# Performance work log

Hardware: AMD Instinct MI355X
Metric: run time of the kernel (lower is better)

## Reference

```python
import jax, jax.numpy as jnp
import numpy as np

B = 64          # batch
N_IN = 1_000_000  # SNPs (n_inputs)
N_OUT = 20_000    # genes (n_outputs = mask.shape[1])
KMAX = 64         # filter_size = max SNPs per gene


def setup_inputs() -> dict:
    key = jax.random.key(0)
    k1, k2, k3, k4 = jax.random.split(key, 4)
    x = jax.random.normal(k1, (B, N_IN), dtype=jnp.float32)
    kernel = jax.random.normal(k2, (KMAX, N_OUT), dtype=jnp.float32) * 0.05
    bias = jnp.zeros((N_OUT, 1), dtype=jnp.float32)
    # static COO mask encoded as padded per-gene index table + valid lengths
    gather_idx = jax.random.randint(k3, (N_OUT, KMAX), 0, N_IN, dtype=jnp.int32)
    lengths = jax.random.randint(k4, (N_OUT,), 1, KMAX + 1, dtype=jnp.int32)
    return {"x": x, "kernel": kernel, "bias": bias,
            "gather_idx": gather_idx, "lengths": lengths}


def reference(x, kernel, bias, gather_idx, lengths):
    # valid[g,k] = 1 if slot k of gene g holds a real SNP (padding mask)
    valid = (jnp.arange(KMAX, dtype=lengths.dtype)[None, :] < lengths[:, None])
    # per-gene weights, zeroed at padded slots: (G, K)
    w = jnp.where(valid, kernel.T, jnp.zeros((), dtype=kernel.dtype))
    # gather inputs per gene group: (B, G, K)
    gathered = x[:, gather_idx]
    # grouped multiply-reduce: (B, G)
    out = jnp.einsum('bgk,gk->bg', gathered, w)
    # bias per (gene, filter), filters = 1 -> output (B, G, 1)
    out = out[..., None] + bias[None, :, :]
    return out  # linear activation
```

## Files before the change

### kernel.cpp

```cpp
#include <hip/hip_runtime.h>
#include <hip/hip_bf16.h>

#define B_DIM 64
#define N_IN 1000000
#define N_OUT 20000
#define KMAX 64
#define GPB 16

__global__ __launch_bounds__(256) void zero_flags(uint4* __restrict__ f) {
    int tid = blockIdx.x * 256 + threadIdx.x;
    if (tid < N_IN / 16) f[tid] = uint4{0, 0, 0, 0};
}

__global__ __launch_bounds__(256) void build_flags(
    const int* __restrict__ gidx, const int* __restrict__ lengths,
    unsigned char* __restrict__ flags) {
    int tid = blockIdx.x * 256 + threadIdx.x;
    int g = tid >> 6, k = tid & 63;
    if (g < N_OUT && k < lengths[g]) flags[gidx[g * KMAX + k]] = 1;
    if (tid == 0) flags[0] = 1;
}

__global__ __launch_bounds__(256) void transpose_x_bf16_masked(
    const float* __restrict__ src, __hip_bfloat16* __restrict__ dst,
    const unsigned char* __restrict__ flags) {
    __shared__ float ldsT[64 * 65];
    __shared__ unsigned char f[64];
    const int t  = threadIdx.x;
    const int c0 = blockIdx.x * 64;
    if (t < 64) f[t] = flags[c0 + t];
    const int col4 = (t & 15) * 4;
    const int r0   = t >> 4;
#pragma unroll
    for (int i = 0; i < 4; ++i) {
        int r = r0 + 16 * i;
        float4 v = *reinterpret_cast<const float4*>(&src[(size_t)r * N_IN + c0 + col4]);
        ldsT[(col4 + 0) * 65 + r] = v.x;
        ldsT[(col4 + 1) * 65 + r] = v.y;
        ldsT[(col4 + 2) * 65 + r] = v.z;
        ldsT[(col4 + 3) * 65 + r] = v.w;
    }
    __syncthreads();
    const int half = t & 31;
    const int cb   = t >> 5;
#pragma unroll
    for (int i = 0; i < 8; ++i) {
        int c = cb + 8 * i;
        if (f[c]) {
            __hip_bfloat162 h2;
            h2.x = __float2bfloat16(ldsT[c * 65 + half * 2]);
            h2.y = __float2bfloat16(ldsT[c * 65 + half * 2 + 1]);
            *reinterpret_cast<__hip_bfloat162*>(&dst[(size_t)(c0 + c) * 64 + half * 2]) = h2;
        }
    }
}

__global__ __launch_bounds__(256) void transpose_64xC_f32(
    const float* __restrict__ src, float* __restrict__ dst, int C) {
    __shared__ float lds[64 * 65];
    const int c0 = blockIdx.x * 64;
    const int t  = threadIdx.x;
    const int cq = t & 63;
    const int rq = t >> 6;
#pragma unroll
    for (int i = 0; i < 16; ++i) {
        int r = i * 4 + rq;
        int c = c0 + cq;
        if (c < C) lds[r * 65 + cq] = src[r * C + c];
    }
    __syncthreads();
#pragma unroll
    for (int i = 0; i < 16; ++i) {
        int c = i * 4 + rq;
        int r = cq;
        if (c0 + c < C) dst[(c0 + c) * 64 + r] = lds[r * 65 + c];
    }
}

__global__ __launch_bounds__(1024) void gather_dot_fused(
    const __hip_bfloat16* __restrict__ xT,
    const float* __restrict__ wT,
    const int*   __restrict__ gidx,
    const int*   __restrict__ lengths,
    const float* __restrict__ bias,
    float*       __restrict__ out) {
    __shared__ float sm[64 * 17];
    const int wave = threadIdx.x >> 6;
    const int lane = threadIdx.x & 63;
    const int g0   = blockIdx.x * GPB;
    const int g    = g0 + wave;

    const int len = lengths[g];
    const int   idx_l = (lane < len) ? gidx[g * KMAX + lane] : 0;
    const float w_l   = (lane < len) ? wT[g * KMAX + lane] : 0.0f;

    float acc = 0.0f;
    for (int k = 0; k < len; k += 4) {
        int   i0 = __shfl(idx_l, k + 0);
        int   i1 = __shfl(idx_l, k + 1);
        int   i2 = __shfl(idx_l, k + 2);
        int   i3 = __shfl(idx_l, k + 3);
        float w0 = __shfl(w_l, k + 0);
        float w1 = __shfl(w_l, k + 1);
        float w2 = __shfl(w_l, k + 2);
        float w3 = __shfl(w_l, k + 3);
        float v0 = __bfloat162float(xT[(size_t)i0 * 64 + lane]);
        float v1 = __bfloat162float(xT[(size_t)i1 * 64 + lane]);
        float v2 = __bfloat162float(xT[(size_t)i2 * 64 + lane]);
        float v3 = __bfloat162float(xT[(size_t)i3 * 64 + lane]);
        acc = fmaf(v0, w0, acc);
        acc = fmaf(v1, w1, acc);
        acc = fmaf(v2, w2, acc);
        acc = fmaf(v3, w3, acc);
    }
    sm[lane * 17 + wave] = acc;
    __syncthreads();
    const int b = threadIdx.x >> 4;
    const int c = threadIdx.x & 15;
    out[(size_t)b * N_OUT + g0 + c] = sm[b * 17 + c] + bias[g0 + c];
}

__global__ __launch_bounds__(256) void direct_kernel(
    const float* __restrict__ x, const float* __restrict__ kern,
    const float* __restrict__ bias, const int* __restrict__ gidx,
    const int* __restrict__ lengths, float* __restrict__ out) {
    const int wave = threadIdx.x >> 6;
    const int lane = threadIdx.x & 63;
    const int g = blockIdx.x * 4 + wave;
    if (g >= N_OUT) return;
    const int len = lengths[g];
    float acc = 0.0f;
    for (int k = 0; k < len; ++k) {
        int   idx = gidx[g * KMAX + k];
        float w   = kern[k * N_OUT + g];
        acc = fmaf(x[(size_t)lane * N_IN + idx], w, acc);
    }
    out[(size_t)lane * N_OUT + g] = acc + bias[g];
}

extern "C" void kernel_launch(void* const* d_in, const int* in_sizes, int n_in,
                              void* d_out, int out_size, void* d_ws, size_t ws_size,
                              hipStream_t stream) {
    const float* x       = (const float*)d_in[0];
    const float* kern    = (const float*)d_in[1];
    const float* bias    = (const float*)d_in[2];
    const int*   gidx    = (const int*)d_in[3];
    const int*   lengths = (const int*)d_in[4];
    float*       out     = (float*)d_out;

    const size_t xT_bytes = (size_t)N_IN * B_DIM * sizeof(__hip_bfloat16);
    const size_t wT_bytes = (size_t)N_OUT * KMAX * sizeof(float);
    const size_t fl_bytes = (size_t)N_IN;

    if (ws_size >= xT_bytes + wT_bytes + fl_bytes) {
        __hip_bfloat16* xT    = (__hip_bfloat16*)d_ws;
        float*          wT    = (float*)((char*)d_ws + xT_bytes);
        unsigned char*  flags = (unsigned char*)((char*)d_ws + xT_bytes + wT_bytes);

        zero_flags<<<(N_IN / 16 + 255) / 256, 256, 0, stream>>>((uint4*)flags);
        build_flags<<<N_OUT * KMAX / 256, 256, 0, stream>>>(gidx, lengths, flags);
        transpose_x_bf16_masked<<<N_IN / 64, 256, 0, stream>>>(x, xT, flags);
        transpose_64xC_f32<<<(N_OUT + 63) / 64, 256, 0, stream>>>(kern, wT, N_OUT);
        gather_dot_fused<<<N_OUT / GPB, 1024, 0, stream>>>(xT, wT, gidx, lengths, bias, out);
    } else {
        direct_kernel<<<N_OUT / 4, 256, 0, stream>>>(x, kern, bias, gidx, lengths, out);
    }
}
```

Measured before the change: 103.9 us.

## Merge flag zeroing with weight transpose, widen bf16 stores and gathers

Folds the flag-zeroing and weight-transpose launches into a single prep kernel, removing one launch. The masked x transpose now writes four bf16 values per thread as an 8-byte store instead of two-element stores. The gather-dot kernel splits each wave into two halves that each handle alternating SNPs, loading two bf16 batch values per 32-bit read and combining the halves with a cross-lane xor shuffle. It unpacks bf16 with bit shifts, cutting the number of gather load instructions at the cost of extra shuffles and a reduction step.

```diff
diff --git a/kernel.cpp b/kernel.cpp
--- a/kernel.cpp
+++ b/kernel.cpp
@@ -7,9 +7,39 @@
 #define KMAX 64
 #define GPB 16
 
-__global__ __launch_bounds__(256) void zero_flags(uint4* __restrict__ f) {
-    int tid = blockIdx.x * 256 + threadIdx.x;
-    if (tid < N_IN / 16) f[tid] = uint4{0, 0, 0, 0};
+__device__ __forceinline__ unsigned short f32_to_bf16_bits(float f) {
+    __hip_bfloat16 b = __float2bfloat16(f);
+    unsigned short s;
+    __builtin_memcpy(&s, &b, sizeof(s));
+    return s;
+}
+
+#define ZERO_BLOCKS 245
+__global__ __launch_bounds__(256) void prep_kernel(
+    uint4* __restrict__ flags4, const float* __restrict__ kern, float* __restrict__ wT) {
+    if (blockIdx.x < ZERO_BLOCKS) {
+        int tid = blockIdx.x * 256 + threadIdx.x;
+        if (tid < N_IN / 16) flags4[tid] = uint4{0, 0, 0, 0};
+        return;
+    }
+    __shared__ float lds[64 * 65];
+    const int c0 = (blockIdx.x - ZERO_BLOCKS) * 64;
+    const int t  = threadIdx.x;
+    const int cq = t & 63;
+    const int rq = t >> 6;
+#pragma unroll
+    for (int i = 0; i < 16; ++i) {
+        int r = i * 4 + rq;
+        int c = c0 + cq;
+        if (c < N_OUT) lds[r * 65 + cq] = kern[r * N_OUT + c];
+    }
+    __syncthreads();
+#pragma unroll
+    for (int i = 0; i < 16; ++i) {
+        int c = i * 4 + rq;
+        int r = cq;
+        if (c0 + c < N_OUT) wT[(c0 + c) * 64 + r] = lds[r * 65 + c];
+    }
 }
 
 __global__ __launch_bounds__(256) void build_flags(
@@ -41,39 +71,19 @@
         ldsT[(col4 + 3) * 65 + r] = v.w;
     }
     __syncthreads();
-    const int half = t & 31;
-    const int cb   = t >> 5;
+    const int m = t & 15;
+    const int cb = t >> 4;
 #pragma unroll
-    for (int i = 0; i < 8; ++i) {
-        int c = cb + 8 * i;
+    for (int i = 0; i < 4; ++i) {
+        int c = cb + 16 * i;
         if (f[c]) {
-            __hip_bfloat162 h2;
-            h2.x = __float2bfloat16(ldsT[c * 65 + half * 2]);
-            h2.y = __float2bfloat16(ldsT[c * 65 + half * 2 + 1]);
-            *reinterpret_cast<__hip_bfloat162*>(&dst[(size_t)(c0 + c) * 64 + half * 2]) = h2;
+            ushort4 h;
+            h.x = f32_to_bf16_bits(ldsT[c * 65 + m * 4 + 0]);
+            h.y = f32_to_bf16_bits(ldsT[c * 65 + m * 4 + 1]);
+            h.z = f32_to_bf16_bits(ldsT[c * 65 + m * 4 + 2]);
+            h.w = f32_to_bf16_bits(ldsT[c * 65 + m * 4 + 3]);
+            *reinterpret_cast<ushort4*>(&dst[(size_t)(c0 + c) * 64 + m * 4]) = h;
         }
-    }
-}
-
-__global__ __launch_bounds__(256) void transpose_64xC_f32(
-    const float* __restrict__ src, float* __restrict__ dst, int C) {
-    __shared__ float lds[64 * 65];
-    const int c0 = blockIdx.x * 64;
-    const int t  = threadIdx.x;
-    const int cq = t & 63;
-    const int rq = t >> 6;
-#pragma unroll
-    for (int i = 0; i < 16; ++i) {
-        int r = i * 4 + rq;
-        int c = c0 + cq;
-        if (c < C) lds[r * 65 + cq] = src[r * C + c];
-    }
-    __syncthreads();
-#pragma unroll
-    for (int i = 0; i < 16; ++i) {
-        int c = i * 4 + rq;
-        int r = cq;
-        if (c0 + c < C) dst[(c0 + c) * 64 + r] = lds[r * 65 + c];
     }
 }
 
@@ -87,6 +97,8 @@
     __shared__ float sm[64 * 17];
     const int wave = threadIdx.x >> 6;
     const int lane = threadIdx.x & 63;
+    const int half = lane >> 5;
+    const int l    = lane & 31;
     const int g0   = blockIdx.x * GPB;
     const int g    = g0 + wave;
 
@@ -94,26 +106,27 @@
     const int   idx_l = (lane < len) ? gidx[g * KMAX + lane] : 0;
     const float w_l   = (lane < len) ? wT[g * KMAX + lane] : 0.0f;
 
-    float acc = 0.0f;
-    for (int k = 0; k < len; k += 4) {
-        int   i0 = __shfl(idx_l, k + 0);
-        int   i1 = __shfl(idx_l, k + 1);
-        int   i2 = __shfl(idx_l, k + 2);
-        int   i3 = __shfl(idx_l, k + 3);
-        float w0 = __shfl(w_l, k + 0);
-        float w1 = __shfl(w_l, k + 1);
-        float w2 = __shfl(w_l, k + 2);
-        float w3 = __shfl(w_l, k + 3);
-        float v0 = __bfloat162float(xT[(size_t)i0 * 64 + lane]);
-        float v1 = __bfloat162float(xT[(size_t)i1 * 64 + lane]);
-        float v2 = __bfloat162float(xT[(size_t)i2 * 64 + lane]);
-        float v3 = __bfloat162float(xT[(size_t)i3 * 64 + lane]);
-        acc = fmaf(v0, w0, acc);
-        acc = fmaf(v1, w1, acc);
-        acc = fmaf(v2, w2, acc);
-        acc = fmaf(v3, w3, acc);
+    float acc0 = 0.0f, acc1 = 0.0f;
+    for (int k = 0; k < len; k += 8) {
+#pragma unroll
+        for (int j = 0; j < 4; ++j) {
+            int   kk  = k + 2 * j + half;
+            int   row = __shfl(idx_l, kk);
+            float w   = __shfl(w_l, kk);
+            unsigned int u = *reinterpret_cast<const unsigned int*>(
+                &xT[(size_t)row * 64 + 2 * l]);
+            float f0 = __uint_as_float(u << 16);
+            float f1 = __uint_as_float(u & 0xFFFF0000u);
+            acc0 = fmaf(f0, w, acc0);
+            acc1 = fmaf(f1, w, acc1);
+        }
     }
-    sm[lane * 17 + wave] = acc;
+    acc0 += __shfl_xor(acc0, 32);
+    acc1 += __shfl_xor(acc1, 32);
+    if (half == 0) {
+        sm[(2 * l + 0) * 17 + wave] = acc0;
+        sm[(2 * l + 1) * 17 + wave] = acc1;
+    }
     __syncthreads();
     const int b = threadIdx.x >> 4;
     const int c = threadIdx.x & 15;
@@ -157,10 +170,10 @@
         float*          wT    = (float*)((char*)d_ws + xT_bytes);
         unsigned char*  flags = (unsigned char*)((char*)d_ws + xT_bytes + wT_bytes);
 
-        zero_flags<<<(N_IN / 16 + 255) / 256, 256, 0, stream>>>((uint4*)flags);
+        prep_kernel<<<ZERO_BLOCKS + (N_OUT + 63) / 64, 256, 0, stream>>>(
+            (uint4*)flags, kern, wT);
         build_flags<<<N_OUT * KMAX / 256, 256, 0, stream>>>(gidx, lengths, flags);
         transpose_x_bf16_masked<<<N_IN / 64, 256, 0, stream>>>(x, xT, flags);
-        transpose_64xC_f32<<<(N_OUT + 63) / 64, 256, 0, stream>>>(kern, wT, N_OUT);
         gather_dot_fused<<<N_OUT / GPB, 1024, 0, stream>>>(xT, wT, gidx, lengths, bias, out);
     } else {
         direct_kernel<<<N_OUT / 4, 256, 0, stream>>>(x, kern, bias, gidx, lengths, out);
```

Result: faster. 91.47 us (-11.9%).
